# Performance work log

Measured on AMD Instinct MI355X. Metric: run time of the kernel, lower is better.

## Reference

```python
import jax, jax.numpy as jnp
import numpy as np
import math

B, S, H, NH = 2, 2048, 2048, 16
HD = H // NH
LAYER_NUMBER = 5
NORM_FACTOR = math.sqrt(HD) * LAYER_NUMBER  # sqrt(head_dim) * coeff
BETA = 1.0 / LAYER_NUMBER
SCALE = float(LAYER_NUMBER)  # ScaledSoftmax scale = coeff
MASK_VALUE = -10000.0


def setup_inputs() -> dict:
    key = jax.random.key(0)
    ks = jax.random.split(key, 6)
    inv_sqrt_h = 1.0 / math.sqrt(H)
    return {
        "hidden_states": jax.random.normal(ks[0], (B, S, H), jnp.float32),
        "alibi": jax.random.normal(ks[1], (NH, 1, S), jnp.float32) * 0.1,
        "w_qkv": jax.random.normal(ks[2], (3 * H, H), jnp.float32) * inv_sqrt_h,
        "b_qkv": jax.random.normal(ks[3], (3 * H,), jnp.float32) * 0.02,
        "w_dense": jax.random.normal(ks[4], (H, H), jnp.float32) * inv_sqrt_h,
        "b_dense": jax.random.normal(ks[5], (H,), jnp.float32) * 0.02,
        "attention_mask": jnp.ones((B, S), jnp.int32),
    }


def reference(hidden_states, alibi, w_qkv, b_qkv, w_dense, b_dense, attention_mask):
    b, s, h = hidden_states.shape
    # QKV projection: [b, s, 3h] -> [b, s, nh, 3*hd] -> split
    mixed = hidden_states @ w_qkv.T + b_qkv
    mixed = mixed.reshape(b, s, NH, 3 * HD)
    q, k, v = jnp.split(mixed, 3, axis=-1)  # each [b, s, nh, hd]

    # Faithful Megatron-style memory reinterpretation (row-major reshape),
    # exactly matching torch's .contiguous().view(s, b*nh, hd).
    q2 = jnp.swapaxes(q.reshape(s, b * NH, HD), 0, 1)  # [b*nh, q_len, hd]
    k2 = jnp.swapaxes(k.reshape(s, b * NH, HD), 0, 1)  # [b*nh, k_len, hd]
    v2 = jnp.swapaxes(v.reshape(s, b * NH, HD), 0, 1)  # [b*nh, k_len, hd]

    # baddbmm: alibi*beta + (q @ k^T)/norm_factor
    alibi_b = jnp.tile(alibi, (b, 1, 1))[: b * NH, :, :s]  # [b*nh, 1, k_len]
    scores = alibi_b * BETA + jnp.einsum("bqd,bkd->bqk", q2, k2) * (1.0 / NORM_FACTOR)
    scores = scores.reshape(b, NH, s, s)

    # ScaledSoftmax: scale then fused causal+padding mask fill, then softmax
    scores = scores * SCALE
    pad_bool = (1 - attention_mask).astype(bool)  # True where padded
    causal = jnp.tril(jnp.ones((s, s), dtype=bool))
    bad = pad_bool[:, None, :, None] | (~causal)[None, None, :, :]  # [b,1,s,s]
    scores = jnp.where(bad, MASK_VALUE, scores)
    probs = jax.nn.softmax(scores, axis=-1)  # [b, nh, s, s]

    # context = probs @ V with the same faithful reshapes
    probs_r = probs.reshape(b * NH, s, s)
    context = jnp.einsum("bqk,bkd->bqd", probs_r, v2)  # [b*nh, q_len, hd]
    context = context.reshape(b, NH, s, HD)
    context = jnp.transpose(context, (2, 0, 1, 3)).reshape(s, b, h)  # [s, b, h]

    out = context @ w_dense.T + b_dense  # [s, b, h]
    return jnp.swapaxes(out, 0, 1)  # [b, s, h]
```

## Files before the change

kernel.cpp:

```cpp
#include <hip/hip_runtime.h>

typedef unsigned short u16;
typedef __bf16  bf16x8 __attribute__((ext_vector_type(8)));
typedef float   f32x4  __attribute__((ext_vector_type(4)));
typedef u16     u16x8  __attribute__((ext_vector_type(8)));
typedef u16     u16x4  __attribute__((ext_vector_type(4)));

#define QSCALE 0.12751744545f

__device__ __forceinline__ u16 f2b(float f) {
    unsigned u = __float_as_uint(f);
    unsigned r = u + 0x7FFFu + ((u >> 16) & 1u);
    return (u16)(r >> 16);
}
__device__ __forceinline__ float b2f(u16 b) {
    return __uint_as_float(((unsigned)b) << 16);
}
__device__ __forceinline__ void async16(const u16* g, u16* l) {
    __builtin_amdgcn_global_load_lds(
        (__attribute__((address_space(1))) void*)(u16*)g,
        (__attribute__((address_space(3))) void*)l, 16, 0, 0);
}

__global__ void cvt_f32_bf16(const float* __restrict__ in, u16* __restrict__ out, int n4) {
    int i = blockIdx.x * blockDim.x + threadIdx.x;
    if (i >= n4) return;
    float4 f = ((const float4*)in)[i];
    u16x4 o;
    o[0] = f2b(f.x); o[1] = f2b(f.y); o[2] = f2b(f.z); o[3] = f2b(f.w);
    *(u16x4*)(out + (size_t)i * 4) = o;
}

__global__ void cvt_wqkv(const float* __restrict__ in, u16* __restrict__ out, int n4) {
    int i = blockIdx.x * blockDim.x + threadIdx.x;
    if (i >= n4) return;
    int row = i >> 9;
    float s = ((row % 384) < 128) ? QSCALE : 1.0f;
    float4 f = ((const float4*)in)[i];
    u16x4 o;
    o[0] = f2b(f.x * s); o[1] = f2b(f.y * s); o[2] = f2b(f.z * s); o[3] = f2b(f.w * s);
    *(u16x4*)(out + (size_t)i * 4) = o;
}

__global__ __launch_bounds__(256) void gemm_bt(
    const u16* __restrict__ A, const u16* __restrict__ B,
    const float* __restrict__ bias, void* __restrict__ C,
    u16* __restrict__ qb, u16* __restrict__ kb, u16* __restrict__ vb,
    int M, int N, int K, int mode)
{
    __shared__ u16 smem[16384];
    u16* As = smem;
    u16* Bs = smem + 8192;

    int tid = threadIdx.x, wave = tid >> 6, lane = tid & 63;
    int lg = lane >> 4, lm = lane & 15;
    int wm = (wave & 1) * 64, wn = (wave >> 1) * 64;

    const u16* Ab = A + (size_t)(blockIdx.y * 128) * K;
    const u16* Bb = B + (size_t)(blockIdx.x * 128) * K;

    f32x4 acc[4][4];
    for (int i = 0; i < 4; i++)
        for (int j = 0; j < 4; j++)
            acc[i][j] = (f32x4){0.f, 0.f, 0.f, 0.f};

    int srow = (lane >> 2), skq = (lane & 3) * 8;

    for (int k0 = 0; k0 < K; k0 += 64) {
        __syncthreads();
        for (int cc = wave; cc < 16; cc += 4) {
            int p = cc >> 3, c = cc & 7;
            int row = c * 16 + srow;
            size_t off = (size_t)row * K + k0 + p * 32 + skq;
            async16(Ab + off, &As[p * 4096 + c * 512]);
            async16(Bb + off, &Bs[p * 4096 + c * 512]);
        }
        __syncthreads();

        for (int p = 0; p < 2; p++) {
            bf16x8 af[4], bf[4];
            for (int i = 0; i < 4; i++) af[i] = *(const bf16x8*)&As[p * 4096 + (wm + i * 16 + lm) * 32 + lg * 8];
            for (int j = 0; j < 4; j++) bf[j] = *(const bf16x8*)&Bs[p * 4096 + (wn + j * 16 + lm) * 32 + lg * 8];
            for (int i = 0; i < 4; i++)
                for (int j = 0; j < 4; j++)
                    acc[i][j] = __builtin_amdgcn_mfma_f32_16x16x32_bf16(af[i], bf[j], acc[i][j], 0, 0, 0);
        }
    }

    if (mode == 1) {
        for (int j = 0; j < 4; j++) {
            int col = blockIdx.x * 128 + wn + j * 16 + lm;
            float bv = bias[col];
            for (int i = 0; i < 4; i++) {
                int row0 = blockIdx.y * 128 + wm + i * 16 + lg * 4;
                for (int r = 0; r < 4; r++) {
                    int row = row0 + r;
                    int orow = ((row & 1) << 11) + (row >> 1);
                    ((float*)C)[(size_t)orow * N + col] = acc[i][j][r] + bv;
                }
            }
        }
        return;
    }

    int ct = blockIdx.x;
    int nh = ct / 3, part = ct - nh * 3;
    float bscale = (part == 0) ? QSCALE : 1.0f;
    int rbase = blockIdx.y * 128;
    int b = rbase >> 11;
    int s0 = rbase & 2047;

    if (part < 2) {
        u16* dst0 = part ? kb : qb;
        for (int j = 0; j < 4; j++) {
            int hd = wn + j * 16 + lm;
            float bv = bias[ct * 128 + hd] * bscale;
            for (int i = 0; i < 4; i++) {
                for (int r = 0; r < 4; r++) {
                    int rl = wm + i * 16 + lg * 4 + r;
                    int s = s0 + rl;
                    int bn = (s & 1) * 16 + nh;
                    int pos = (b << 10) + (s >> 1);
                    dst0[((size_t)(bn * 2048 + pos)) * 128 + hd] = f2b(acc[i][j][r] + bv);
                }
            }
        }
    } else {
        u16 (*arr)[64][128] = (u16(*)[64][128])smem;
        __syncthreads();
        for (int j = 0; j < 4; j++) {
            int hd = wn + j * 16 + lm;
            float bv = bias[ct * 128 + hd];
            for (int i = 0; i < 4; i++) {
                for (int r = 0; r < 4; r++) {
                    int rl = wm + i * 16 + lg * 4 + r;
                    arr[rl & 1][rl >> 1][hd] = f2b(acc[i][j][r] + bv);
                }
            }
        }
        __syncthreads();
        int hd = tid & 127, par = tid >> 7;
        int bn = par * 16 + nh;
        int pos0 = (b << 10) + (s0 >> 1);
        u16* dst = vb + ((size_t)(bn * 128 + hd)) * 2048 + pos0;
        for (int c = 0; c < 8; c++) {
            u16x8 w;
            for (int e = 0; e < 8; e++) w[e] = arr[par][c * 8 + e][hd];
            *(u16x8*)(dst + c * 8) = w;
        }
    }
}

__global__ __launch_bounds__(256) void attn(
    const u16* __restrict__ qb, const u16* __restrict__ kb,
    const u16* __restrict__ vb, const float* __restrict__ alibi,
    u16* __restrict__ ctx)
{
    __shared__ u16 Ks[64 * 136];
    __shared__ u16 Vt[128 * 88];
    __shared__ u16 Ps[4][16 * 72];

    int bn = blockIdx.y;
    int tid = threadIdx.x, wave = tid >> 6, lane = tid & 63;
    int lg = lane >> 4, lm = lane & 15;

    const float* al = alibi + (bn & 15) * 2048;

    int krow = tid >> 2, kq = (tid & 3) * 32;
    int vhd  = tid >> 1, vh2 = (tid & 1) * 32;
    const u16* ksrc0 = kb + (size_t)(bn * 2048 + krow) * 128 + kq;
    const u16* vsrc0 = vb + (size_t)(bn * 128 + vhd) * 2048 + vh2;

    u16* ps = &Ps[wave][0];
    bf16x8 ones;
    {
        u16x8 t;
        for (int j = 0; j < 8; j++) t[j] = 0x3F80;
        ones = *(bf16x8*)&t;
    }

    for (int pass = 0; pass < 2; pass++) {
        int qt = pass ? (31 - blockIdx.x) : blockIdx.x;
        int q0 = qt * 64;

        bf16x8 qf[4];
        {
            const u16* qp = qb + ((size_t)bn * 2048 + q0 + wave * 16 + lm) * 128 + lg * 8;
            for (int kc = 0; kc < 4; kc++) qf[kc] = *(const bf16x8*)(qp + kc * 32);
        }

        f32x4 o[9];
        for (int i = 0; i < 9; i++) o[i] = (f32x4){0.f, 0.f, 0.f, 0.f};

        u16x8 kreg[4], vreg[4];
        for (int i = 0; i < 4; i++) kreg[i] = *(const u16x8*)(ksrc0 + i * 8);
        for (int i = 0; i < 4; i++) vreg[i] = *(const u16x8*)(vsrc0 + i * 8);

        for (int kt = 0; kt <= qt; kt++) {
            int k0 = kt * 64;
            __syncthreads();
            {
                u16* d1 = &Ks[krow * 136 + kq];
                for (int i = 0; i < 4; i++) *(u16x8*)(d1 + i * 8) = kreg[i];
                u16* d2 = &Vt[vhd * 88 + vh2];
                for (int i = 0; i < 4; i++) *(u16x8*)(d2 + i * 8) = vreg[i];
            }
            __syncthreads();

            if (kt < qt) {
                const u16* s1 = ksrc0 + (size_t)(kt + 1) * 64 * 128;
                const u16* s2 = vsrc0 + (kt + 1) * 64;
                for (int i = 0; i < 4; i++) kreg[i] = *(const u16x8*)(s1 + i * 8);
                for (int i = 0; i < 4; i++) vreg[i] = *(const u16x8*)(s2 + i * 8);
            }

            f32x4 sc[4];
            for (int tc = 0; tc < 4; tc++) {
                const u16* kr = &Ks[(tc * 16 + lm) * 136 + lg * 8];
                f32x4 a = (f32x4){0.f, 0.f, 0.f, 0.f};
                for (int kc = 0; kc < 4; kc++)
                    a = __builtin_amdgcn_mfma_f32_16x16x32_bf16(qf[kc], *(const bf16x8*)(kr + kc * 32), a, 0, 0, 0);
                sc[tc] = a;
            }

            bool diag = (kt == qt);
            for (int tc = 0; tc < 4; tc++) {
                int kg = k0 + tc * 16 + lm;
                float av = (al[kg] - 8.0f) * 1.4426950408889634f;
                for (int r = 0; r < 4; r++) {
                    float v = sc[tc][r] + av;
                    if (diag && kg > q0 + wave * 16 + lg * 4 + r) v = -3e38f;
                    ps[(lg * 4 + r) * 72 + tc * 16 + lm] = f2b(__builtin_amdgcn_exp2f(v));
                }
            }

            for (int kc = 0; kc < 2; kc++) {
                bf16x8 pf = *(const bf16x8*)&ps[lm * 72 + kc * 32 + lg * 8];
                for (int i = 0; i < 8; i++) {
                    bf16x8 vf = *(const bf16x8*)&Vt[(i * 16 + lm) * 88 + kc * 32 + lg * 8];
                    o[i] = __builtin_amdgcn_mfma_f32_16x16x32_bf16(pf, vf, o[i], 0, 0, 0);
                }
                o[8] = __builtin_amdgcn_mfma_f32_16x16x32_bf16(pf, ones, o[8], 0, 0, 0);
            }
        }

        for (int r = 0; r < 4; r++) {
            float inv = 1.0f / o[8][r];
            int qg = q0 + wave * 16 + lg * 4 + r;
            int row = qg * 2 + (bn >> 4);
            u16* crow = ctx + (size_t)row * 2048 + (bn & 15) * 128 + lm;
            for (int i = 0; i < 8; i++)
                crow[i * 16] = f2b(o[i][r] * inv);
        }
    }
}

extern "C" void kernel_launch(void* const* d_in, const int* in_sizes, int n_in,
                              void* d_out, int out_size, void* d_ws, size_t ws_size,
                              hipStream_t stream)
{
    const float* hs    = (const float*)d_in[0];
    const float* alibi = (const float*)d_in[1];
    const float* wqkv  = (const float*)d_in[2];
    const float* bqkv  = (const float*)d_in[3];
    const float* wd    = (const float*)d_in[4];
    const float* bd    = (const float*)d_in[5];
    float* out = (float*)d_out;

    char* ws = (char*)d_ws;
    u16* wqkv_b = (u16*)(ws + 0);
    u16* hs_b   = (u16*)(ws + 25165824);
    u16* ctx    = (u16*)(ws + 41943040);
    u16* wd_b   = wqkv_b;
    u16* qb     = (u16*)(ws + 92274688);
    u16* kb     = (u16*)(ws + 109051904);
    u16* vb     = (u16*)(ws + 125829120);

    cvt_f32_bf16<<<8192,  256, 0, stream>>>(hs,   hs_b,   2097152);
    cvt_wqkv   <<<12288, 256, 0, stream>>>(wqkv, wqkv_b, 3145728);

    gemm_bt<<<dim3(48, 32), 256, 0, stream>>>(hs_b, wqkv_b, bqkv, nullptr,
                                              qb, kb, vb, 4096, 6144, 2048, 0);

    cvt_f32_bf16<<<4096, 256, 0, stream>>>(wd, wd_b, 1048576);

    attn<<<dim3(16, 32), 256, 0, stream>>>(qb, kb, vb, alibi, ctx);

    gemm_bt<<<dim3(16, 32), 256, 0, stream>>>(ctx, wd_b, bd, out,
                                              nullptr, nullptr, nullptr, 4096, 2048, 2048, 1);
}
```

Baseline: 396.6 us.

## Add 256x256-tile QKV GEMM with 4-stage async LDS pipeline

Replaces the generic 128x128 GEMM for the QKV projection with a dedicated kernel that uses 256x256 output tiles, 512 threads and a four-slot async global-to-LDS ring with XOR-swizzled layout and split MFMA phases. The larger tile raises arithmetic intensity and the deeper prefetch is meant to hide global load latency. The epilogue scatters Q/K directly and transposes V through LDS. The cost is 128KB of LDS and heavy register use per block, and only 384 blocks for the grid.

Measured after the change: 403.8 us. About the same (+1.8%).

```diff
diff --git a/kernel.cpp b/kernel.cpp
--- a/kernel.cpp
+++ b/kernel.cpp
@@ -40,6 +40,132 @@
     u16x4 o;
     o[0] = f2b(f.x * s); o[1] = f2b(f.y * s); o[2] = f2b(f.z * s); o[3] = f2b(f.w * s);
     *(u16x4*)(out + (size_t)i * 4) = o;
+}
+
+__global__ __launch_bounds__(512, 2) void gemm_qkv(
+    const u16* __restrict__ A, const u16* __restrict__ B,
+    const float* __restrict__ bias,
+    u16* __restrict__ qb, u16* __restrict__ kb, u16* __restrict__ vb)
+{
+    constexpr int K  = 2048;
+    constexpr int NS = K / 32;
+    __shared__ u16 lds[65536];
+
+    const int tid = threadIdx.x, wave = tid >> 6, lane = tid & 63;
+    const int lm = lane & 15, lg = lane >> 4;
+    const int wr = wave >> 2, wc = wave & 3;
+
+    const int rbase = blockIdx.y * 256;
+    const int cbase = blockIdx.x * 256;
+
+    const int srl = lane >> 2;
+    const int scs = ((lane & 3) ^ ((lane >> 3) & 3)) << 3;
+    const u16* sl0;
+    int lbase;
+    {
+        int qq = (wave & 3) * 4;
+        if (wave < 4) { sl0 = A + (size_t)rbase * K; lbase = qq * 512; }
+        else          { sl0 = B + (size_t)cbase * K; lbase = 8192 + qq * 512; }
+        sl0 += (size_t)(qq * 16 + srl) * K + scs;
+    }
+    auto stage2 = [&](int s_, int c0) {
+        int slot = (s_ & 3) * 16384;
+        size_t k0 = (size_t)s_ * 32;
+        for (int c = c0; c < c0 + 2; c++)
+            async16(sl0 + (size_t)c * 16 * K + k0, &lds[slot + lbase + c * 512]);
+    };
+
+    const int coff = (lg ^ ((lm >> 1) & 3)) << 3;
+    const int aoff = (wr * 128 + lm) * 32 + coff;
+    const int boff = 8192 + (wc * 64 + lm) * 32 + coff;
+
+    f32x4 acc[8][4];
+    for (int m = 0; m < 8; m++)
+        for (int n = 0; n < 4; n++)
+            acc[m][n] = (f32x4){0.f, 0.f, 0.f, 0.f};
+
+    stage2(0, 0); stage2(0, 2);
+    stage2(1, 0); stage2(1, 2);
+    stage2(2, 0); stage2(2, 2);
+    asm volatile("s_waitcnt vmcnt(8)" ::: "memory");
+    __builtin_amdgcn_s_barrier();
+
+    for (int s = 0; s < NS; s++) {
+        const u16* sl = &lds[(s & 3) * 16384];
+        bf16x8 af[4], bf[4];
+
+        for (int n = 0; n < 4; n++) bf[n] = *(const bf16x8*)&sl[boff + n * 512];
+        for (int m = 0; m < 4; m++) af[m] = *(const bf16x8*)&sl[aoff + m * 512];
+        if (s + 3 < NS) stage2(s + 3, 0);
+        __builtin_amdgcn_s_barrier();
+        __builtin_amdgcn_s_setprio(1);
+        for (int m = 0; m < 4; m++)
+            for (int n = 0; n < 4; n++)
+                acc[m][n] = __builtin_amdgcn_mfma_f32_16x16x32_bf16(af[m], bf[n], acc[m][n], 0, 0, 0);
+        __builtin_amdgcn_s_setprio(0);
+        __builtin_amdgcn_s_barrier();
+
+        for (int m = 0; m < 4; m++) af[m] = *(const bf16x8*)&sl[aoff + (m + 4) * 512];
+        if (s + 3 < NS) stage2(s + 3, 2);
+        __builtin_amdgcn_s_barrier();
+        __builtin_amdgcn_s_setprio(1);
+        for (int m = 0; m < 4; m++)
+            for (int n = 0; n < 4; n++)
+                acc[m + 4][n] = __builtin_amdgcn_mfma_f32_16x16x32_bf16(af[m], bf[n], acc[m + 4][n], 0, 0, 0);
+        __builtin_amdgcn_s_setprio(0);
+
+        if (s + 1 < NS) {
+            if (s < NS - 3)       asm volatile("s_waitcnt vmcnt(8)" ::: "memory");
+            else if (s == NS - 3) asm volatile("s_waitcnt vmcnt(4)" ::: "memory");
+            else                  asm volatile("s_waitcnt vmcnt(0)" ::: "memory");
+            __builtin_amdgcn_s_barrier();
+        }
+    }
+
+    __syncthreads();
+
+    const int ct   = (cbase >> 7) + (wc >> 1);
+    const int nh   = ct / 3, part = ct - nh * 3;
+    const int hd0  = (wc & 1) * 64;
+    const int posb = (rbase >> 11) << 10;
+    const int sblk = (rbase & 2047) + wr * 128;
+
+    if (part < 2) {
+        u16* dst0 = part ? kb : qb;
+        const float bsc = part ? 1.0f : QSCALE;
+        for (int n = 0; n < 4; n++) {
+            int hd = hd0 + n * 16 + lm;
+            float bv = bias[ct * 128 + hd] * bsc;
+            for (int m = 0; m < 8; m++) {
+                for (int r = 0; r < 4; r++) {
+                    int s_  = sblk + m * 16 + lg * 4 + r;
+                    int bn  = (s_ & 1) * 16 + nh;
+                    int pos = posb + (s_ >> 1);
+                    dst0[((size_t)(bn * 2048 + pos)) * 128 + hd] = f2b(acc[m][n][r] + bv);
+                }
+            }
+        }
+    } else {
+        u16* scr = &lds[wave * 8192];
+        for (int n = 0; n < 4; n++) {
+            int hdl = n * 16 + lm;
+            float bv = bias[ct * 128 + hd0 + hdl];
+            for (int m = 0; m < 8; m++)
+                for (int r = 0; r < 4; r++)
+                    scr[(m * 16 + lg * 4 + r) * 64 + hdl] = f2b(acc[m][n][r] + bv);
+        }
+        int pos0 = posb + (sblk >> 1);
+        for (int par = 0; par < 2; par++) {
+            int bn = par * 16 + nh;
+            u16* dst = vb + ((size_t)(bn * 128 + hd0 + lane)) * 2048 + pos0;
+            for (int p8 = 0; p8 < 8; p8++) {
+                u16x8 w;
+                for (int e = 0; e < 8; e++)
+                    w[e] = scr[(2 * (p8 * 8 + e) + par) * 64 + lane];
+                *(u16x8*)(dst + p8 * 8) = w;
+            }
+        }
+    }
 }
 
 __global__ __launch_bounds__(256) void gemm_bt(
@@ -279,8 +405,7 @@
     cvt_f32_bf16<<<8192,  256, 0, stream>>>(hs,   hs_b,   2097152);
     cvt_wqkv   <<<12288, 256, 0, stream>>>(wqkv, wqkv_b, 3145728);
 
-    gemm_bt<<<dim3(48, 32), 256, 0, stream>>>(hs_b, wqkv_b, bqkv, nullptr,
-                                              qb, kb, vb, 4096, 6144, 2048, 0);
+    gemm_qkv<<<dim3(24, 16), 512, 0, stream>>>(hs_b, wqkv_b, bqkv, qb, kb, vb);
 
     cvt_f32_bf16<<<4096, 256, 0, stream>>>(wd, wd_b, 1048576);
 
```
